# Kernel tuning notes

Hardware: AMD Instinct MI355X
Metric: run time of the kernel (lower is better)

The kernel has to match this reference:

```python
import jax, jax.numpy as jnp
import numpy as np

Q_HEADS, KV_HEADS, HEAD_SIZE, H, MAX_LEN = 16, 4, 64, 1024, 4096
B, S = 1, 4096


def _rope_tables(max_len, head_size):
    half = head_size // 2
    inv_freq = 1.0 / (10000.0 ** (np.arange(half, dtype=np.float32) / half))
    pos = np.arange(max_len, dtype=np.float32)
    ang = pos[:, None] * inv_freq[None, :]  # [max_len, half]
    return jnp.asarray(np.sin(ang)), jnp.asarray(np.cos(ang))


def setup_inputs() -> dict:
    key = jax.random.key(0)
    ks = jax.random.split(key, 6)
    sc = 1.0 / np.sqrt(H)
    x = jax.random.normal(ks[0], (B, S, H), dtype=jnp.float32)
    wq = jax.random.normal(ks[1], (H, H), dtype=jnp.float32) * sc
    wk = jax.random.normal(ks[2], (H, KV_HEADS * HEAD_SIZE), dtype=jnp.float32) * sc
    wv = jax.random.normal(ks[3], (H, KV_HEADS * HEAD_SIZE), dtype=jnp.float32) * sc
    wo = jax.random.normal(ks[4], (H, H), dtype=jnp.float32) * sc
    sin, cos = _rope_tables(MAX_LEN, HEAD_SIZE)
    full_mask = jnp.tril(jnp.ones((MAX_LEN, MAX_LEN), dtype=bool))
    attention_mask = jnp.ones((B, S), dtype=jnp.int32)
    return {"x": x, "attention_mask": attention_mask, "start": 0,
            "wq": wq, "wk": wk, "wv": wv, "wo": wo,
            "sin": sin, "cos": cos, "full_mask": full_mask}


def _rotate(t, sin, cos, start):
    # t: [b, heads, s, head_size]; interleaved even/odd RoPE
    s = t.shape[2]
    sn = sin[start:start + s, :][None, None, :, :]
    cs = cos[start:start + s, :][None, None, :, :]
    even, odd = t[..., 0::2], t[..., 1::2]
    out_even = cs * even - sn * odd
    out_odd = sn * even + cs * odd
    return jnp.stack((out_even, out_odd), axis=-1).reshape(t.shape)


def _expand_kv(t, group):
    # [b, kv_heads, s, d] -> [b, kv_heads*group, s, d]
    b, kvh, s, d = t.shape
    return jnp.broadcast_to(t[:, :, None], (b, kvh, group, s, d)).reshape(b, kvh * group, s, d)


def reference(x, attention_mask, start, wq, wk, wv, wo, sin, cos, full_mask):
    b, s, _ = x.shape
    group = Q_HEADS // KV_HEADS
    Q = (x @ wq).reshape(b, s, Q_HEADS, HEAD_SIZE).transpose(0, 2, 1, 3)
    K = (x @ wk).reshape(b, s, KV_HEADS, HEAD_SIZE).transpose(0, 2, 1, 3)
    V = (x @ wv).reshape(b, s, KV_HEADS, HEAD_SIZE).transpose(0, 2, 1, 3)
    Q = _rotate(Q, sin, cos, start)
    K = _rotate(K, sin, cos, start)
    K = _expand_kv(K, group)
    V = _expand_kv(V, group)
    z = jnp.einsum('bhqd,bhkd->bhqk', Q, K) / (HEAD_SIZE ** 0.5)
    kv_len = start + s
    mask = full_mask[:s, :kv_len][None, None, :, :]
    amask = (attention_mask[:, :kv_len] != 0)[:, None, None, :]
    mask = mask & amask
    z = jnp.where(mask, z, -1000000.0)
    A = jax.nn.softmax(z, axis=-1)
    ctx = jnp.einsum('bhqk,bhkd->bhqd', A, V)
    q_mask = attention_mask[:, :s].astype(ctx.dtype)[:, None, :, None]
    ctx = ctx * q_mask
    ctx = ctx.transpose(0, 2, 1, 3).reshape(b, s, H)
    return ctx @ wo
```

## Files before the change

kernel.cpp:

```cpp
#include <hip/hip_runtime.h>

typedef __bf16 bf16x8 __attribute__((ext_vector_type(8)));
typedef float f32x4 __attribute__((ext_vector_type(4)));
typedef unsigned int u32x4 __attribute__((ext_vector_type(4)));

typedef const void __attribute__((address_space(1)))* gas1;
typedef void __attribute__((address_space(3)))* las3;

__device__ __forceinline__ unsigned short f2bf(float f) {
  unsigned int u = __builtin_bit_cast(unsigned int, f);
  u += 0x7fffu + ((u >> 16) & 1u);
  return (unsigned short)(u >> 16);
}
__device__ __forceinline__ float bf2f(unsigned short h) {
  unsigned int u = ((unsigned int)h) << 16;
  return __builtin_bit_cast(float, u);
}
__device__ __forceinline__ unsigned int pack2bf(float lo, float hi) {
  return (unsigned int)f2bf(lo) | ((unsigned int)f2bf(hi) << 16);
}
__device__ __forceinline__ unsigned int packtr(float lo, float hi) {
  return __builtin_amdgcn_perm(__builtin_bit_cast(unsigned int, hi),
                               __builtin_bit_cast(unsigned int, lo), 0x07060302u);
}

__global__ __launch_bounds__(256) void prep(const float* __restrict__ x,
                                            const float* __restrict__ wq,
                                            const float* __restrict__ wk,
                                            const float* __restrict__ wv,
                                            const float* __restrict__ wo,
                                            unsigned short* __restrict__ xb,
                                            unsigned short* __restrict__ wtqkv,
                                            unsigned short* __restrict__ wot) {
  __shared__ float tile[32][33];
  const int b = blockIdx.x;
  const int tid = threadIdx.x;
  if (b < 4096) {
    int i = b * 256 + tid;
    float4 v = ((const float4*)x)[i];
    uint2 o;
    o.x = pack2bf(v.x, v.y);
    o.y = pack2bf(v.z, v.w);
    ((uint2*)xb)[i] = o;
    return;
  }
  const float* src;
  unsigned short* dst;
  int R, C, t;
  if (b < 5120)      { t = b - 4096; src = wq; dst = wtqkv;               R = 1024; C = 1024; }
  else if (b < 5376) { t = b - 5120; src = wk; dst = wtqkv + 1024 * 1024; R = 1024; C = 256; }
  else if (b < 5632) { t = b - 5376; src = wv; dst = wtqkv + 1280 * 1024; R = 1024; C = 256; }
  else               { t = b - 5632; src = wo; dst = wot;                 R = 1024; C = 1024; }
  const int ntc = C >> 5;
  const int c0 = (t % ntc) * 32, r0 = (t / ntc) * 32;
  const int tx = tid & 31, ty = tid >> 5;
#pragma unroll
  for (int i = 0; i < 4; ++i)
    tile[ty + i * 8][tx] = src[(r0 + ty + i * 8) * C + c0 + tx];
  __syncthreads();
#pragma unroll
  for (int i = 0; i < 4; ++i)
    dst[(c0 + ty + i * 8) * R + r0 + tx] = f2bf(tile[tx][ty + i * 8]);
}

__global__ __launch_bounds__(256, 2) void gemm_qkv(const unsigned short* __restrict__ A,
                                                   const unsigned short* __restrict__ Bt,
                                                   const float* __restrict__ sinT,
                                                   const float* __restrict__ cosT,
                                                   unsigned short* __restrict__ Qh,
                                                   unsigned short* __restrict__ Kh,
                                                   unsigned short* __restrict__ Vt) {
  __shared__ __align__(16) unsigned short Als[2][128 * 32];
  __shared__ __align__(16) unsigned short Bls[2][128 * 32];
  const int K = 1024;
  const int tid = threadIdx.x;
  const int wave = tid >> 6, lane = tid & 63;
  const int lgrp = lane >> 4, lmod = lane & 15;
  const int wm = (wave & 1) * 64, wn = (wave >> 1) * 64;
  const int m0 = blockIdx.y * 128, n0 = blockIdx.x * 128;

  f32x4 acc[4][4] = {};

  for (int k0 = 0; k0 < K; k0 += 64) {
    __syncthreads();
#pragma unroll
    for (int half = 0; half < 2; ++half) {
      int kk = k0 + half * 32;
#pragma unroll
      for (int it = 0; it < 2; ++it) {
        int idx = tid + it * 256;
        int rr = idx >> 2, cc = (idx & 3) * 8;
        __builtin_amdgcn_global_load_lds((gas1)(const void*)&A[(size_t)(m0 + rr) * K + kk + cc],
                                         (las3)(void*)&Als[half][(it * 256 + wave * 64) * 8], 16, 0, 0);
        __builtin_amdgcn_global_load_lds((gas1)(const void*)&Bt[(size_t)(n0 + rr) * K + kk + cc],
                                         (las3)(void*)&Bls[half][(it * 256 + wave * 64) * 8], 16, 0, 0);
      }
    }
    __syncthreads();
#pragma unroll
    for (int half = 0; half < 2; ++half) {
      bf16x8 af[4], bfr[4];
#pragma unroll
      for (int mi = 0; mi < 4; ++mi)
        af[mi] = __builtin_bit_cast(bf16x8, *(const u32x4*)&Als[half][(wm + mi * 16 + lmod) * 32 + lgrp * 8]);
#pragma unroll
      for (int ni = 0; ni < 4; ++ni)
        bfr[ni] = __builtin_bit_cast(bf16x8, *(const u32x4*)&Bls[half][(wn + ni * 16 + lmod) * 32 + lgrp * 8]);
#pragma unroll
      for (int mi = 0; mi < 4; ++mi)
#pragma unroll
        for (int ni = 0; ni < 4; ++ni)
          acc[mi][ni] = __builtin_amdgcn_mfma_f32_16x16x32_bf16(af[mi], bfr[ni], acc[mi][ni], 0, 0, 0);
    }
  }

  const int cbase = n0 + wn;
  if (cbase >= 1280) {
    const int kvh = (cbase - 1280) >> 6;
#pragma unroll
    for (int mi = 0; mi < 4; ++mi)
#pragma unroll
      for (int ni = 0; ni < 4; ++ni) {
        int d = ni * 16 + lmod;
        int s = m0 + wm + mi * 16 + lgrp * 4;
        uint2 o;
        o.x = pack2bf(acc[mi][ni][0], acc[mi][ni][1]);
        o.y = pack2bf(acc[mi][ni][2], acc[mi][ni][3]);
        *(uint2*)&Vt[((size_t)(kvh * 64 + d)) * 4096 + s] = o;
      }
    return;
  }

  __syncthreads();
  float* sinls = (float*)&Als[0][0];
  float* cosls = (float*)&Bls[0][0];
#pragma unroll
  for (int j = 0; j < 4; ++j) {
    int idx = tid + j * 256;
    int rr = idx >> 3, cc = (idx & 7) * 4;
    *(float4*)&sinls[rr * 32 + cc] = *(const float4*)&sinT[(size_t)(m0 + rr) * 32 + cc];
    *(float4*)&cosls[rr * 32 + cc] = *(const float4*)&cosT[(size_t)(m0 + rr) * 32 + cc];
  }
  __syncthreads();

  const float qscale = 0.18033688011112042f;
  const bool isQ = (cbase < 1024);
  const int h = isQ ? (cbase >> 6) : ((cbase - 1024) >> 6);
  unsigned short* dstbase = isQ ? Qh : Kh;
  const bool evn = (lmod & 1) == 0;
#pragma unroll
  for (int mi = 0; mi < 4; ++mi)
#pragma unroll
    for (int ni = 0; ni < 4; ++ni) {
      int d = ni * 16 + lmod;
      int i = ni * 8 + (lmod >> 1);
#pragma unroll
      for (int r = 0; r < 4; ++r) {
        float v = acc[mi][ni][r];
        float p = __shfl_xor(v, 1, 64);
        int rl = wm + mi * 16 + lgrp * 4 + r;
        float sn = sinls[rl * 32 + i], cs = cosls[rl * 32 + i];
        float e = evn ? v : p, o = evn ? p : v;
        float outv = evn ? (cs * e - sn * o) : (sn * e + cs * o);
        if (isQ) outv *= qscale;
        dstbase[((size_t)h * 4096 + m0 + rl) * 64 + d] = f2bf(outv);
      }
    }
}

__global__ __launch_bounds__(256, 2) void gemm_out(const unsigned short* __restrict__ A,
                                                   const unsigned short* __restrict__ Bt,
                                                   float* __restrict__ Cout) {
  __shared__ __align__(16) unsigned short Als[2][128 * 32];
  __shared__ __align__(16) unsigned short Bls[2][128 * 32];
  const int K = 1024, N = 1024;
  const int tid = threadIdx.x;
  const int wave = tid >> 6, lane = tid & 63;
  const int lgrp = lane >> 4, lmod = lane & 15;
  const int wm = (wave & 1) * 64, wn = (wave >> 1) * 64;
  const int m0 = blockIdx.y * 128, n0 = blockIdx.x * 128;

  f32x4 acc[4][4] = {};

  for (int k0 = 0; k0 < K; k0 += 64) {
    __syncthreads();
#pragma unroll
    for (int half = 0; half < 2; ++half) {
      int kk = k0 + half * 32;
#pragma unroll
      for (int it = 0; it < 2; ++it) {
        int idx = tid + it * 256;
        int rr = idx >> 2, cc = (idx & 3) * 8;
        __builtin_amdgcn_global_load_lds((gas1)(const void*)&A[(size_t)(m0 + rr) * K + kk + cc],
                                         (las3)(void*)&Als[half][(it * 256 + wave * 64) * 8], 16, 0, 0);
        __builtin_amdgcn_global_load_lds((gas1)(const void*)&Bt[(size_t)(n0 + rr) * K + kk + cc],
                                         (las3)(void*)&Bls[half][(it * 256 + wave * 64) * 8], 16, 0, 0);
      }
    }
    __syncthreads();
#pragma unroll
    for (int half = 0; half < 2; ++half) {
      bf16x8 af[4], bfr[4];
#pragma unroll
      for (int mi = 0; mi < 4; ++mi)
        af[mi] = __builtin_bit_cast(bf16x8, *(const u32x4*)&Als[half][(wm + mi * 16 + lmod) * 32 + lgrp * 8]);
#pragma unroll
      for (int ni = 0; ni < 4; ++ni)
        bfr[ni] = __builtin_bit_cast(bf16x8, *(const u32x4*)&Bls[half][(wn + ni * 16 + lmod) * 32 + lgrp * 8]);
#pragma unroll
      for (int mi = 0; mi < 4; ++mi)
#pragma unroll
        for (int ni = 0; ni < 4; ++ni)
          acc[mi][ni] = __builtin_amdgcn_mfma_f32_16x16x32_bf16(af[mi], bfr[ni], acc[mi][ni], 0, 0, 0);
    }
  }

#pragma unroll
  for (int mi = 0; mi < 4; ++mi)
#pragma unroll
    for (int ni = 0; ni < 4; ++ni)
#pragma unroll
      for (int r = 0; r < 4; ++r) {
        int row = m0 + wm + mi * 16 + lgrp * 4 + r;
        int col = n0 + wn + ni * 16 + lmod;
        Cout[(size_t)row * N + col] = acc[mi][ni][r];
      }
}

__global__ __launch_bounds__(256, 2) void attn5(const unsigned short* __restrict__ Qh,
                                                const unsigned short* __restrict__ Kh,
                                                const unsigned short* __restrict__ Vt,
                                                unsigned short* __restrict__ ctx) {
  __shared__ __align__(16) unsigned short Kls[8 * 128 * 8];
  __shared__ __align__(16) unsigned short Vls[64 * 136];
  const int bx = blockIdx.x;
  const int head = bx & 15;
  const int qidx = bx >> 4;
  const int qb = (qidx < 16) ? (31 - qidx) : (qidx - 16);
  const int kvh = head >> 2;
  const int tid = threadIdx.x;
  const int wave = tid >> 6, lane = tid & 63;
  const int lgrp = lane >> 4, lmod = lane & 15;
  const int qbase = qb * 128;

  const unsigned short* Kg = Kh + (size_t)kvh * 4096 * 64;
  const unsigned short* Vg = Vt + (size_t)kvh * 64 * 4096;

  bf16x8 qf[2][2];
  int qrow[2];
#pragma unroll
  for (int qt = 0; qt < 2; ++qt) {
    qrow[qt] = qbase + wave * 32 + qt * 16 + lmod;
    const unsigned short* Qg = Qh + ((size_t)head * 4096 + qrow[qt]) * 64;
    qf[qt][0] = __builtin_bit_cast(bf16x8, *(const u32x4*)&Qg[lgrp * 8]);
    qf[qt][1] = __builtin_bit_cast(bf16x8, *(const u32x4*)&Qg[32 + lgrp * 8]);
  }

  int krd[2];
#pragma unroll
  for (int h = 0; h < 2; ++h)
    krd[h] = (h * 64 + lgrp * 16 + (lmod ^ (h * 4 + lgrp))) * 8;
  const int vbase = lmod * 136 + lgrp * 8;

  f32x4 accO[2][4] = {};
  float m_i[2] = {-3e38f, -3e38f}, l_i[2] = {0.f, 0.f};

  for (int kc = 0; kc <= qb; ++kc) {
    const int kb = kc * 128;
    __syncthreads();
#pragma unroll
    for (int i = 0; i < 4; ++i) {
      int ii = tid + i * 256;
      int r = ii >> 3, s8 = ii & 7;
      u32x4 dK = *(const u32x4*)&Kg[(size_t)(kb + r) * 64 + s8 * 8];
      int g = r >> 5, r5 = r & 31;
      int t = (r5 >> 2) & 1;
      int m = ((r5 >> 3) << 2) | (r5 & 3);
      int sigma = ((s8 >> 2) << 6) | ((s8 & 3) << 4) | (m ^ s8);
      *(u32x4*)&Kls[(((g << 1) | t) << 10) + (sigma << 3)] = dK;
    }
#pragma unroll
    for (int i = 0; i < 4; ++i) {
      int ii = tid + i * 256;
      int r = ii >> 4, sg = (ii & 15) * 8;
      *(u32x4*)&Vls[r * 136 + sg] = *(const u32x4*)&Vg[(size_t)r * 4096 + kb + sg];
    }
    __syncthreads();

    f32x4 s[4][2][2];
#pragma unroll
    for (int g = 0; g < 4; ++g)
#pragma unroll
      for (int t = 0; t < 2; ++t) {
        int tb = ((g << 1) | t) << 10;
        bf16x8 alo = __builtin_bit_cast(bf16x8, *(const u32x4*)&Kls[tb + krd[0]]);
        bf16x8 ahi = __builtin_bit_cast(bf16x8, *(const u32x4*)&Kls[tb + krd[1]]);
#pragma unroll
        for (int qt = 0; qt < 2; ++qt) {
          f32x4 z = {};
          z = __builtin_amdgcn_mfma_f32_16x16x32_bf16(alo, qf[qt][0], z, 0, 0, 0);
          z = __builtin_amdgcn_mfma_f32_16x16x32_bf16(ahi, qf[qt][1], z, 0, 0, 0);
          s[g][t][qt] = z;
        }
      }

#pragma unroll
    for (int qt = 0; qt < 2; ++qt) {
      if (kb + 127 > qbase + wave * 32 + qt * 16) {
#pragma unroll
        for (int g = 0; g < 4; ++g)
#pragma unroll
          for (int t = 0; t < 2; ++t)
#pragma unroll
            for (int r = 0; r < 4; ++r) {
              int key = kb + 32 * g + 8 * lgrp + 4 * t + r;
              if (key > qrow[qt]) s[g][t][qt][r] = -3e38f;
            }
      }
    }

#pragma unroll
    for (int qt = 0; qt < 2; ++qt) {
      f32x4 v0 = s[0][0][qt], v1 = s[0][1][qt];
#pragma unroll
      for (int g = 1; g < 4; ++g)
#pragma unroll
        for (int r = 0; r < 4; ++r) {
          v0[r] = fmaxf(v0[r], s[g][0][qt][r]);
          v1[r] = fmaxf(v1[r], s[g][1][qt][r]);
        }
      float mx = fmaxf(fmaxf(fmaxf(v0[0], v0[1]), fmaxf(v0[2], v0[3])),
                       fmaxf(fmaxf(v1[0], v1[1]), fmaxf(v1[2], v1[3])));
      mx = fmaxf(mx, __shfl_xor(mx, 16, 64));
      mx = fmaxf(mx, __shfl_xor(mx, 32, 64));
      float mnew = fmaxf(m_i[qt], mx);
      float alpha = __builtin_amdgcn_exp2f(m_i[qt] - mnew);
      m_i[qt] = mnew;
      f32x4 su = {};
#pragma unroll
      for (int g = 0; g < 4; ++g)
#pragma unroll
        for (int t = 0; t < 2; ++t)
#pragma unroll
          for (int r = 0; r < 4; ++r) {
            float ev = __builtin_amdgcn_exp2f(s[g][t][qt][r] - mnew);
            s[g][t][qt][r] = ev;
            su[r] += ev;
          }
      float rs = (su[0] + su[1]) + (su[2] + su[3]);
      rs += __shfl_xor(rs, 16, 64);
      rs += __shfl_xor(rs, 32, 64);
      l_i[qt] = l_i[qt] * alpha + rs;
#pragma unroll
      for (int dt = 0; dt < 4; ++dt)
#pragma unroll
        for (int r = 0; r < 4; ++r) accO[qt][dt][r] *= alpha;
    }

#pragma unroll
    for (int g = 0; g < 4; ++g) {
      bf16x8 pf[2];
#pragma unroll
      for (int qt = 0; qt < 2; ++qt) {
        u32x4 pk;
        pk[0] = packtr(s[g][0][qt][0], s[g][0][qt][1]);
        pk[1] = packtr(s[g][0][qt][2], s[g][0][qt][3]);
        pk[2] = packtr(s[g][1][qt][0], s[g][1][qt][1]);
        pk[3] = packtr(s[g][1][qt][2], s[g][1][qt][3]);
        pf[qt] = __builtin_bit_cast(bf16x8, pk);
      }
#pragma unroll
      for (int dt = 0; dt < 4; ++dt) {
        bf16x8 vf = __builtin_bit_cast(bf16x8, *(const u32x4*)&Vls[vbase + dt * 2176 + 32 * g]);
        accO[0][dt] = __builtin_amdgcn_mfma_f32_16x16x32_bf16(vf, pf[0], accO[0][dt], 0, 0, 0);
        accO[1][dt] = __builtin_amdgcn_mfma_f32_16x16x32_bf16(vf, pf[1], accO[1][dt], 0, 0, 0);
      }
    }
  }

#pragma unroll
  for (int qt = 0; qt < 2; ++qt) {
    float inv = 1.f / l_i[qt];
#pragma unroll
    for (int dt = 0; dt < 4; ++dt) {
      uint2 o;
      o.x = pack2bf(accO[qt][dt][0] * inv, accO[qt][dt][1] * inv);
      o.y = pack2bf(accO[qt][dt][2] * inv, accO[qt][dt][3] * inv);
      *(uint2*)&ctx[(size_t)qrow[qt] * 1024 + head * 64 + dt * 16 + lgrp * 4] = o;
    }
  }
}

extern "C" void kernel_launch(void* const* d_in, const int* in_sizes, int n_in,
                              void* d_out, int out_size, void* d_ws, size_t ws_size,
                              hipStream_t stream) {
  const float* x    = (const float*)d_in[0];
  const float* wq   = (const float*)d_in[3];
  const float* wk   = (const float*)d_in[4];
  const float* wv   = (const float*)d_in[5];
  const float* wo   = (const float*)d_in[6];
  const float* sinT = (const float*)d_in[7];
  const float* cosT = (const float*)d_in[8];

  unsigned short* ws    = (unsigned short*)d_ws;
  unsigned short* xb    = ws;
  unsigned short* wtqkv = xb + 4096 * 1024;
  unsigned short* wot   = wtqkv + 1536 * 1024;
  unsigned short* Qh    = wot + 1024 * 1024;
  unsigned short* Kh    = Qh + 16 * 4096 * 64;
  unsigned short* Vt    = Kh + 4 * 4096 * 64;
  unsigned short* ctx   = Vt + 4 * 64 * 4096;
  float* out = (float*)d_out;

  prep<<<6656, 256, 0, stream>>>(x, wq, wk, wv, wo, xb, wtqkv, wot);
  gemm_qkv<<<dim3(12, 32), 256, 0, stream>>>(xb, wtqkv, sinT, cosT, Qh, Kh, Vt);
  attn5<<<dim3(512), 256, 0, stream>>>(Qh, Kh, Vt, ctx);
  gemm_out<<<dim3(8, 32), 256, 0, stream>>>(ctx, wot, out);
}
```

Before: 251.0 us.

## Double-buffer LDS tiles in both GEMMs and attention to overlap loads with MFMA

Both GEMM kernels now prefetch the next 32-wide K slice into the alternate LDS buffer with global_load_lds while computing on the current one, which cuts the per-iteration syncs from two to one. The attention kernel adds double-buffered K/V tiles: the next tile is prefetched into registers during compute and written to the other LDS buffer afterwards. It also replaces the swizzled K layout with a padded row layout (stride 68) read through 8-byte LDS loads. The cost is more LDS per block, more registers in attention, and possible bank conflicts from the new K layout.

Result: no change. 250.0 us (-0.4%).

```diff
diff --git a/kernel.cpp b/kernel.cpp
--- a/kernel.cpp
+++ b/kernel.cpp
@@ -78,40 +78,47 @@
   const int lgrp = lane >> 4, lmod = lane & 15;
   const int wm = (wave & 1) * 64, wn = (wave >> 1) * 64;
   const int m0 = blockIdx.y * 128, n0 = blockIdx.x * 128;
+  const int rr0 = tid >> 2, cc0 = (tid & 3) * 8;
+  const int rr1 = (tid + 256) >> 2, cc1 = cc0;
 
   f32x4 acc[4][4] = {};
 
-  for (int k0 = 0; k0 < K; k0 += 64) {
+  __builtin_amdgcn_global_load_lds((gas1)(const void*)&A[(size_t)(m0 + rr0) * K + cc0],
+                                   (las3)(void*)&Als[0][(wave * 64) * 8], 16, 0, 0);
+  __builtin_amdgcn_global_load_lds((gas1)(const void*)&Bt[(size_t)(n0 + rr0) * K + cc0],
+                                   (las3)(void*)&Bls[0][(wave * 64) * 8], 16, 0, 0);
+  __builtin_amdgcn_global_load_lds((gas1)(const void*)&A[(size_t)(m0 + rr1) * K + cc1],
+                                   (las3)(void*)&Als[0][(256 + wave * 64) * 8], 16, 0, 0);
+  __builtin_amdgcn_global_load_lds((gas1)(const void*)&Bt[(size_t)(n0 + rr1) * K + cc1],
+                                   (las3)(void*)&Bls[0][(256 + wave * 64) * 8], 16, 0, 0);
+  __syncthreads();
+
+  int p = 0;
+  for (int k0 = 0; k0 < K; k0 += 32, p ^= 1) {
+    if (k0 + 32 < K) {
+      int kk = k0 + 32;
+      __builtin_amdgcn_global_load_lds((gas1)(const void*)&A[(size_t)(m0 + rr0) * K + kk + cc0],
+                                       (las3)(void*)&Als[p ^ 1][(wave * 64) * 8], 16, 0, 0);
+      __builtin_amdgcn_global_load_lds((gas1)(const void*)&Bt[(size_t)(n0 + rr0) * K + kk + cc0],
+                                       (las3)(void*)&Bls[p ^ 1][(wave * 64) * 8], 16, 0, 0);
+      __builtin_amdgcn_global_load_lds((gas1)(const void*)&A[(size_t)(m0 + rr1) * K + kk + cc1],
+                                       (las3)(void*)&Als[p ^ 1][(256 + wave * 64) * 8], 16, 0, 0);
+      __builtin_amdgcn_global_load_lds((gas1)(const void*)&Bt[(size_t)(n0 + rr1) * K + kk + cc1],
+                                       (las3)(void*)&Bls[p ^ 1][(256 + wave * 64) * 8], 16, 0, 0);
+    }
+    bf16x8 af[4], bfr[4];
+#pragma unroll
+    for (int mi = 0; mi < 4; ++mi)
+      af[mi] = __builtin_bit_cast(bf16x8, *(const u32x4*)&Als[p][(wm + mi * 16 + lmod) * 32 + lgrp * 8]);
+#pragma unroll
+    for (int ni = 0; ni < 4; ++ni)
+      bfr[ni] = __builtin_bit_cast(bf16x8, *(const u32x4*)&Bls[p][(wn + ni * 16 + lmod) * 32 + lgrp * 8]);
+#pragma unroll
+    for (int mi = 0; mi < 4; ++mi)
+#pragma unroll
+      for (int ni = 0; ni < 4; ++ni)
+        acc[mi][ni] = __builtin_amdgcn_mfma_f32_16x16x32_bf16(af[mi], bfr[ni], acc[mi][ni], 0, 0, 0);
     __syncthreads();
-#pragma unroll
-    for (int half = 0; half < 2; ++half) {
-      int kk = k0 + half * 32;
-#pragma unroll
-      for (int it = 0; it < 2; ++it) {
-        int idx = tid + it * 256;
-        int rr = idx >> 2, cc = (idx & 3) * 8;
-        __builtin_amdgcn_global_load_lds((gas1)(const void*)&A[(size_t)(m0 + rr) * K + kk + cc],
-                                         (las3)(void*)&Als[half][(it * 256 + wave * 64) * 8], 16, 0, 0);
-        __builtin_amdgcn_global_load_lds((gas1)(const void*)&Bt[(size_t)(n0 + rr) * K + kk + cc],
-                                         (las3)(void*)&Bls[half][(it * 256 + wave * 64) * 8], 16, 0, 0);
-      }
-    }
-    __syncthreads();
-#pragma unroll
-    for (int half = 0; half < 2; ++half) {
-      bf16x8 af[4], bfr[4];
-#pragma unroll
-      for (int mi = 0; mi < 4; ++mi)
-        af[mi] = __builtin_bit_cast(bf16x8, *(const u32x4*)&Als[half][(wm + mi * 16 + lmod) * 32 + lgrp * 8]);
-#pragma unroll
-      for (int ni = 0; ni < 4; ++ni)
-        bfr[ni] = __builtin_bit_cast(bf16x8, *(const u32x4*)&Bls[half][(wn + ni * 16 + lmod) * 32 + lgrp * 8]);
-#pragma unroll
-      for (int mi = 0; mi < 4; ++mi)
-#pragma unroll
-        for (int ni = 0; ni < 4; ++ni)
-          acc[mi][ni] = __builtin_amdgcn_mfma_f32_16x16x32_bf16(af[mi], bfr[ni], acc[mi][ni], 0, 0, 0);
-    }
   }
 
   const int cbase = n0 + wn;
@@ -131,7 +138,6 @@
     return;
   }
 
-  __syncthreads();
   float* sinls = (float*)&Als[0][0];
   float* cosls = (float*)&Bls[0][0];
 #pragma unroll
@@ -157,10 +163,10 @@
 #pragma unroll
       for (int r = 0; r < 4; ++r) {
         float v = acc[mi][ni][r];
-        float p = __shfl_xor(v, 1, 64);
+        float pp = __shfl_xor(v, 1, 64);
         int rl = wm + mi * 16 + lgrp * 4 + r;
         float sn = sinls[rl * 32 + i], cs = cosls[rl * 32 + i];
-        float e = evn ? v : p, o = evn ? p : v;
+        float e = evn ? v : pp, o = evn ? pp : v;
         float outv = evn ? (cs * e - sn * o) : (sn * e + cs * o);
         if (isQ) outv *= qscale;
         dstbase[((size_t)h * 4096 + m0 + rl) * 64 + d] = f2bf(outv);
@@ -179,40 +185,47 @@
   const int lgrp = lane >> 4, lmod = lane & 15;
   const int wm = (wave & 1) * 64, wn = (wave >> 1) * 64;
   const int m0 = blockIdx.y * 128, n0 = blockIdx.x * 128;
+  const int rr0 = tid >> 2, cc0 = (tid & 3) * 8;
+  const int rr1 = (tid + 256) >> 2, cc1 = cc0;
 
   f32x4 acc[4][4] = {};
 
-  for (int k0 = 0; k0 < K; k0 += 64) {
+  __builtin_amdgcn_global_load_lds((gas1)(const void*)&A[(size_t)(m0 + rr0) * K + cc0],
+                                   (las3)(void*)&Als[0][(wave * 64) * 8], 16, 0, 0);
+  __builtin_amdgcn_global_load_lds((gas1)(const void*)&Bt[(size_t)(n0 + rr0) * K + cc0],
+                                   (las3)(void*)&Bls[0][(wave * 64) * 8], 16, 0, 0);
+  __builtin_amdgcn_global_load_lds((gas1)(const void*)&A[(size_t)(m0 + rr1) * K + cc1],
+                                   (las3)(void*)&Als[0][(256 + wave * 64) * 8], 16, 0, 0);
+  __builtin_amdgcn_global_load_lds((gas1)(const void*)&Bt[(size_t)(n0 + rr1) * K + cc1],
+                                   (las3)(void*)&Bls[0][(256 + wave * 64) * 8], 16, 0, 0);
+  __syncthreads();
+
+  int p = 0;
+  for (int k0 = 0; k0 < K; k0 += 32, p ^= 1) {
+    if (k0 + 32 < K) {
+      int kk = k0 + 32;
+      __builtin_amdgcn_global_load_lds((gas1)(const void*)&A[(size_t)(m0 + rr0) * K + kk + cc0],
+                                       (las3)(void*)&Als[p ^ 1][(wave * 64) * 8], 16, 0, 0);
+      __builtin_amdgcn_global_load_lds((gas1)(const void*)&Bt[(size_t)(n0 + rr0) * K + kk + cc0],
+                                       (las3)(void*)&Bls[p ^ 1][(wave * 64) * 8], 16, 0, 0);
+      __builtin_amdgcn_global_load_lds((gas1)(const void*)&A[(size_t)(m0 + rr1) * K + kk + cc1],
+                                       (las3)(void*)&Als[p ^ 1][(256 + wave * 64) * 8], 16, 0, 0);
+      __builtin_amdgcn_global_load_lds((gas1)(const void*)&Bt[(size_t)(n0 + rr1) * K + kk + cc1],
+                                       (las3)(void*)&Bls[p ^ 1][(256 + wave * 64) * 8], 16, 0, 0);
+    }
+    bf16x8 af[4], bfr[4];
+#pragma unroll
+    for (int mi = 0; mi < 4; ++mi)
+      af[mi] = __builtin_bit_cast(bf16x8, *(const u32x4*)&Als[p][(wm + mi * 16 + lmod) * 32 + lgrp * 8]);
+#pragma unroll
+    for (int ni = 0; ni < 4; ++ni)
+      bfr[ni] = __builtin_bit_cast(bf16x8, *(const u32x4*)&Bls[p][(wn + ni * 16 + lmod) * 32 + lgrp * 8]);
+#pragma unroll
+    for (int mi = 0; mi < 4; ++mi)
+#pragma unroll
+      for (int ni = 0; ni < 4; ++ni)
+        acc[mi][ni] = __builtin_amdgcn_mfma_f32_16x16x32_bf16(af[mi], bfr[ni], acc[mi][ni], 0, 0, 0);
     __syncthreads();
-#pragma unroll
-    for (int half = 0; half < 2; ++half) {
-      int kk = k0 + half * 32;
-#pragma unroll
-      for (int it = 0; it < 2; ++it) {
-        int idx = tid + it * 256;
-        int rr = idx >> 2, cc = (idx & 3) * 8;
-        __builtin_amdgcn_global_load_lds((gas1)(const void*)&A[(size_t)(m0 + rr) * K + kk + cc],
-                                         (las3)(void*)&Als[half][(it * 256 + wave * 64) * 8], 16, 0, 0);
-        __builtin_amdgcn_global_load_lds((gas1)(const void*)&Bt[(size_t)(n0 + rr) * K + kk + cc],
-                                         (las3)(void*)&Bls[half][(it * 256 + wave * 64) * 8], 16, 0, 0);
-      }
-    }
-    __syncthreads();
-#pragma unroll
-    for (int half = 0; half < 2; ++half) {
-      bf16x8 af[4], bfr[4];
-#pragma unroll
-      for (int mi = 0; mi < 4; ++mi)
-        af[mi] = __builtin_bit_cast(bf16x8, *(const u32x4*)&Als[half][(wm + mi * 16 + lmod) * 32 + lgrp * 8]);
-#pragma unroll
-      for (int ni = 0; ni < 4; ++ni)
-        bfr[ni] = __builtin_bit_cast(bf16x8, *(const u32x4*)&Bls[half][(wn + ni * 16 + lmod) * 32 + lgrp * 8]);
-#pragma unroll
-      for (int mi = 0; mi < 4; ++mi)
-#pragma unroll
-        for (int ni = 0; ni < 4; ++ni)
-          acc[mi][ni] = __builtin_amdgcn_mfma_f32_16x16x32_bf16(af[mi], bfr[ni], acc[mi][ni], 0, 0, 0);
-    }
   }
 
 #pragma unroll
@@ -227,12 +240,12 @@
       }
 }
 
-__global__ __launch_bounds__(256, 2) void attn5(const unsigned short* __restrict__ Qh,
+__global__ __launch_bounds__(256, 2) void attn6(const unsigned short* __restrict__ Qh,
                                                 const unsigned short* __restrict__ Kh,
                                                 const unsigned short* __restrict__ Vt,
                                                 unsigned short* __restrict__ ctx) {
-  __shared__ __align__(16) unsigned short Kls[8 * 128 * 8];
-  __shared__ __align__(16) unsigned short Vls[64 * 136];
+  __shared__ __align__(16) unsigned short Kls[2][128 * 68];
+  __shared__ __align__(16) unsigned short Vls[2][64 * 136];
   const int bx = blockIdx.x;
   const int head = bx & 15;
   const int qidx = bx >> 4;
@@ -256,45 +269,60 @@
     qf[qt][1] = __builtin_bit_cast(bf16x8, *(const u32x4*)&Qg[32 + lgrp * 8]);
   }
 
-  int krd[2];
-#pragma unroll
-  for (int h = 0; h < 2; ++h)
-    krd[h] = (h * 64 + lgrp * 16 + (lmod ^ (h * 4 + lgrp))) * 8;
+  const int kbase = (8 * (lmod >> 2) + (lmod & 3)) * 68 + lgrp * 8;
   const int vbase = lmod * 136 + lgrp * 8;
+
+  const int kr = tid >> 3, ks = (tid & 7) * 8;
+  const int vr = tid >> 4, vs = (tid & 15) * 8;
 
   f32x4 accO[2][4] = {};
   float m_i[2] = {-3e38f, -3e38f}, l_i[2] = {0.f, 0.f};
 
-  for (int kc = 0; kc <= qb; ++kc) {
+  u32x4 kreg[4], vreg[4];
+#pragma unroll
+  for (int i = 0; i < 4; ++i) {
+    int ii = tid + i * 256;
+    kreg[i] = *(const u32x4*)&Kg[(size_t)(ii >> 3) * 64 + (ii & 7) * 8];
+    vreg[i] = *(const u32x4*)&Vg[(size_t)(ii >> 4) * 4096 + (ii & 15) * 8];
+  }
+#pragma unroll
+  for (int i = 0; i < 4; ++i) {
+    int ii = tid + i * 256;
+    uint2* pd = (uint2*)&Kls[0][(ii >> 3) * 68 + (ii & 7) * 8];
+    pd[0] = make_uint2(kreg[i][0], kreg[i][1]);
+    pd[1] = make_uint2(kreg[i][2], kreg[i][3]);
+    *(u32x4*)&Vls[0][(ii >> 4) * 136 + (ii & 15) * 8] = vreg[i];
+  }
+  __syncthreads();
+
+  int p = 0;
+  for (int kc = 0; kc <= qb; ++kc, p ^= 1) {
     const int kb = kc * 128;
-    __syncthreads();
-#pragma unroll
-    for (int i = 0; i < 4; ++i) {
-      int ii = tid + i * 256;
-      int r = ii >> 3, s8 = ii & 7;
-      u32x4 dK = *(const u32x4*)&Kg[(size_t)(kb + r) * 64 + s8 * 8];
-      int g = r >> 5, r5 = r & 31;
-      int t = (r5 >> 2) & 1;
-      int m = ((r5 >> 3) << 2) | (r5 & 3);
-      int sigma = ((s8 >> 2) << 6) | ((s8 & 3) << 4) | (m ^ s8);
-      *(u32x4*)&Kls[(((g << 1) | t) << 10) + (sigma << 3)] = dK;
-    }
-#pragma unroll
-    for (int i = 0; i < 4; ++i) {
-      int ii = tid + i * 256;
-      int r = ii >> 4, sg = (ii & 15) * 8;
-      *(u32x4*)&Vls[r * 136 + sg] = *(const u32x4*)&Vg[(size_t)r * 4096 + kb + sg];
-    }
-    __syncthreads();
+    const bool hasNext = (kc < qb);
+    if (hasNext) {
+      const int nb = kb + 128;
+#pragma unroll
+      for (int i = 0; i < 4; ++i) {
+        int ii = tid + i * 256;
+        kreg[i] = *(const u32x4*)&Kg[(size_t)(nb + (ii >> 3)) * 64 + (ii & 7) * 8];
+        vreg[i] = *(const u32x4*)&Vg[(size_t)(ii >> 4) * 4096 + nb + (ii & 15) * 8];
+      }
+    }
 
     f32x4 s[4][2][2];
 #pragma unroll
     for (int g = 0; g < 4; ++g)
 #pragma unroll
       for (int t = 0; t < 2; ++t) {
-        int tb = ((g << 1) | t) << 10;
-        bf16x8 alo = __builtin_bit_cast(bf16x8, *(const u32x4*)&Kls[tb + krd[0]]);
-        bf16x8 ahi = __builtin_bit_cast(bf16x8, *(const u32x4*)&Kls[tb + krd[1]]);
+        const unsigned short* ka = &Kls[p][kbase + (32 * g + 4 * t) * 68];
+        uint2 a0 = *(const uint2*)&ka[0];
+        uint2 a1 = *(const uint2*)&ka[4];
+        uint2 b0 = *(const uint2*)&ka[32];
+        uint2 b1 = *(const uint2*)&ka[36];
+        u32x4 lo = {a0.x, a0.y, a1.x, a1.y};
+        u32x4 hi = {b0.x, b0.y, b1.x, b1.y};
+        bf16x8 alo = __builtin_bit_cast(bf16x8, lo);
+        bf16x8 ahi = __builtin_bit_cast(bf16x8, hi);
 #pragma unroll
         for (int qt = 0; qt < 2; ++qt) {
           f32x4 z = {};
@@ -371,11 +399,23 @@
       }
 #pragma unroll
       for (int dt = 0; dt < 4; ++dt) {
-        bf16x8 vf = __builtin_bit_cast(bf16x8, *(const u32x4*)&Vls[vbase + dt * 2176 + 32 * g]);
+        bf16x8 vf = __builtin_bit_cast(bf16x8, *(const u32x4*)&Vls[p][vbase + dt * 2176 + 32 * g]);
         accO[0][dt] = __builtin_amdgcn_mfma_f32_16x16x32_bf16(vf, pf[0], accO[0][dt], 0, 0, 0);
         accO[1][dt] = __builtin_amdgcn_mfma_f32_16x16x32_bf16(vf, pf[1], accO[1][dt], 0, 0, 0);
       }
     }
+
+    if (hasNext) {
+#pragma unroll
+      for (int i = 0; i < 4; ++i) {
+        int ii = tid + i * 256;
+        uint2* pd = (uint2*)&Kls[p ^ 1][(ii >> 3) * 68 + (ii & 7) * 8];
+        pd[0] = make_uint2(kreg[i][0], kreg[i][1]);
+        pd[1] = make_uint2(kreg[i][2], kreg[i][3]);
+        *(u32x4*)&Vls[p ^ 1][(ii >> 4) * 136 + (ii & 15) * 8] = vreg[i];
+      }
+    }
+    __syncthreads();
   }
 
 #pragma unroll
@@ -414,6 +454,6 @@
 
   prep<<<6656, 256, 0, stream>>>(x, wq, wk, wv, wo, xb, wtqkv, wot);
   gemm_qkv<<<dim3(12, 32), 256, 0, stream>>>(xb, wtqkv, sinT, cosT, Qh, Kh, Vt);
-  attn5<<<dim3(512), 256, 0, stream>>>(Qh, Kh, Vt, ctx);
+  attn6<<<dim3(512), 256, 0, stream>>>(Qh, Kh, Vt, ctx);
   gemm_out<<<dim3(8, 32), 256, 0, stream>>>(ctx, wot, out);
 }
```
